# Performance work log

Hardware: AMD Instinct MI355X
Metric: run time of the kernel (lower is better)

## Reference

```python
import jax, jax.numpy as jnp
import numpy as np
import math

NUM_BANDS = 16
BINS = 1024
CROPSIZE = 1024
BATCH = 4


def setup_inputs() -> dict:
    key = jax.random.key(0)
    ks = jax.random.split(key, 10)
    s = 1.0 / math.sqrt(BINS)
    return {
        "x": jax.random.normal(ks[0], (BATCH, CROPSIZE, BINS), jnp.float32),
        "Wq": jax.random.normal(ks[1], (BINS, BINS), jnp.float32) * s,
        "bq": jax.random.normal(ks[2], (BINS,), jnp.float32) * 0.02,
        "Wk": jax.random.normal(ks[3], (BINS, BINS), jnp.float32) * s,
        "bk": jax.random.normal(ks[4], (BINS,), jnp.float32) * 0.02,
        "Wv": jax.random.normal(ks[5], (BINS, BINS), jnp.float32) * s,
        "bv": jax.random.normal(ks[6], (BINS,), jnp.float32) * 0.02,
        "Wo": jax.random.normal(ks[7], (BINS, BINS), jnp.float32) * s,
        "bo": jax.random.normal(ks[8], (BINS,), jnp.float32) * 0.02,
        "er": jax.random.normal(ks[9], (BINS // NUM_BANDS, CROPSIZE), jnp.float32),
    }


def reference(x, Wq, bq, Wk, bk, Wv, bv, Wo, bo, er):
    b, w, c = x.shape
    h = NUM_BANDS
    d = c // h
    # Linear projections (torch Linear: x @ W.T + b)
    q = (jnp.einsum("bwc,oc->bwo", x, Wq) + bq).reshape(b, w, h, d).transpose(0, 2, 1, 3)  # [b,h,w,d]
    k = (jnp.einsum("bwc,oc->bwo", x, Wk) + bk).reshape(b, w, h, d).transpose(0, 2, 1, 3)  # [b,h,w,d]
    v = (jnp.einsum("bwc,oc->bwo", x, Wv) + bv).reshape(b, w, h, d).transpose(0, 2, 1, 3)  # [b,h,w,d]
    # relative-position bias via skew trick
    qe = jnp.einsum("bhwd,dc->bhwc", q, er)  # [b,h,w,cropsize]
    qe = jnp.pad(qe, ((0, 0), (0, 0), (0, 0), (1, 0)))  # pad last dim on left -> [b,h,w,crop+1]
    p = jnp.swapaxes(qe, 2, 3)[:, :, 1:, :]  # [b,h,crop,w] == [b,h,w,w] since crop==w
    qk = (jnp.einsum("bhwd,bhud->bhwu", q, k) + p) / math.sqrt(c)
    a = jax.nn.softmax(qk, axis=-1)
    av = jnp.einsum("bhwu,bhud->bhwd", a, v).transpose(0, 2, 1, 3).reshape(b, w, c)
    return jnp.einsum("bwc,oc->bwo", av, Wo) + bo
```

## Files before the change

kernel.cpp:

```cpp
#include <hip/hip_runtime.h>
#include <stdint.h>

typedef __attribute__((ext_vector_type(8))) short   short8;
typedef __attribute__((ext_vector_type(8))) __bf16  bf16x8;
typedef __attribute__((ext_vector_type(4))) float   floatx4;

__device__ __forceinline__ float bf2f(uint16_t h) {
    union { uint32_t u; float f; } v; v.u = ((uint32_t)h) << 16; return v.f;
}
__device__ __forceinline__ uint16_t f2bf(float f) {
    union { float f; uint32_t u; } v; v.f = f;
    uint32_t u = v.u;
    u += 0x7FFFu + ((u >> 16) & 1u);
    return (uint16_t)(u >> 16);
}
__device__ __forceinline__ floatx4 mfma16(short8 a, short8 b, floatx4 c) {
    return __builtin_amdgcn_mfma_f32_16x16x32_bf16(
        __builtin_bit_cast(bf16x8, a), __builtin_bit_cast(bf16x8, b), c, 0, 0, 0);
}
__device__ __forceinline__ void gll16(const short* g, short* l) {
    __builtin_amdgcn_global_load_lds(
        (const __attribute__((address_space(1))) uint32_t*)g,
        (__attribute__((address_space(3))) uint32_t*)l, 16, 0, 0);
}

__global__ void conv_all(
    const float* __restrict__ x,
    const float* __restrict__ Wq, const float* __restrict__ Wk,
    const float* __restrict__ Wv, const float* __restrict__ Wo,
    const float* __restrict__ bq, const float* __restrict__ bk,
    const float* __restrict__ bv, const float* __restrict__ bo,
    const float* __restrict__ er,
    short* __restrict__ xb, short* __restrict__ Wb,
    short* __restrict__ ball, short* __restrict__ ErT)
{
    int blk = blockIdx.x, tid = threadIdx.x;
    if (blk < 4096) {
        int i = blk * 256 + tid;
        float4 v = ((const float4*)x)[i];
        ((short4*)xb)[i] = make_short4((short)f2bf(v.x), (short)f2bf(v.y),
                                       (short)f2bf(v.z), (short)f2bf(v.w));
    } else if (blk < 8192) {
        int rel = blk - 4096;
        int wsel = rel >> 10;
        int i = (rel & 1023) * 256 + tid;
        const float* W = (wsel == 0) ? Wq : (wsel == 1) ? Wk : (wsel == 2) ? Wv : Wo;
        float4 v = ((const float4*)W)[i];
        ((short4*)(Wb + ((size_t)wsel << 20)))[i] =
            make_short4((short)f2bf(v.x), (short)f2bf(v.y),
                        (short)f2bf(v.z), (short)f2bf(v.w));
    } else if (blk < 8448) {
        int idx = (blk - 8192) * 256 + tid;
        int w = idx >> 6, d = idx & 63;
        ErT[idx] = (short)f2bf(er[d * 1024 + w]);
    } else {
        int idx = (blk - 8448) * 256 + tid;
        int sel = idx >> 10, j = idx & 1023;
        const float* s = (sel == 0) ? bq : (sel == 1) ? bk : (sel == 2) ? bv : bo;
        ball[idx] = (short)f2bf(s[j]);
    }
}

__device__ __forceinline__ void gemm_body(
    const short* __restrict__ A, const short* __restrict__ Wt,
    const short* __restrict__ bias, short* __restrict__ dst,
    float* __restrict__ dstf, int variant)
{
    __shared__ short As[128 * 64];
    __shared__ short Bs[128 * 64];
    const int tid  = threadIdx.x;
    const int wid  = tid >> 6;
    const int lane = tid & 63;
    const int m0 = blockIdx.x * 128;
    const int n0 = blockIdx.y * 128;
    const int wm = (wid >> 1) * 64;
    const int wn = (wid & 1) * 64;
    const int lrow = lane & 15;
    const int quad = lane >> 4;
    const int srow = lane >> 3;
    const int sscol = (((lane & 7) ^ (srow & 7)) << 3);
    const int rx = lrow & 7;

    floatx4 acc[4][4];
#pragma unroll
    for (int r = 0; r < 4; ++r)
#pragma unroll
        for (int c = 0; c < 4; ++c) acc[r][c] = (floatx4){0.f, 0.f, 0.f, 0.f};

    for (int k0 = 0; k0 < 1024; k0 += 64) {
#pragma unroll
        for (int i = 0; i < 4; ++i) {
            int q = wid * 4 + i;
            gll16(A + (size_t)(m0 + q * 8 + srow) * 1024 + k0 + sscol,
                  &As[q * 512 + lane * 8]);
        }
#pragma unroll
        for (int i = 0; i < 4; ++i) {
            int q = wid * 4 + i;
            gll16(Wt + (size_t)(n0 + q * 8 + srow) * 1024 + k0 + sscol,
                  &Bs[q * 512 + lane * 8]);
        }
        __syncthreads();
#pragma unroll
        for (int ks = 0; ks < 2; ++ks) {
            short8 af[4], bfr[4];
#pragma unroll
            for (int r = 0; r < 4; ++r)
                af[r] = *(const short8*)&As[(wm + r * 16 + lrow) * 64 +
                                            (((ks * 4 + quad) ^ rx) << 3)];
#pragma unroll
            for (int c = 0; c < 4; ++c)
                bfr[c] = *(const short8*)&Bs[(wn + c * 16 + lrow) * 64 +
                                             (((ks * 4 + quad) ^ rx) << 3)];
#pragma unroll
            for (int r = 0; r < 4; ++r)
#pragma unroll
                for (int c = 0; c < 4; ++c)
                    acc[r][c] = mfma16(af[r], bfr[c], acc[r][c]);
        }
        __syncthreads();
    }

#pragma unroll
    for (int c = 0; c < 4; ++c) {
        int col = n0 + wn + c * 16 + lrow;
        float bv = bf2f((uint16_t)bias[col]);
#pragma unroll
        for (int r = 0; r < 4; ++r) {
#pragma unroll
            for (int g = 0; g < 4; ++g) {
                int m = m0 + wm + r * 16 + quad * 4 + g;
                float fv = acc[r][c][g] + bv;
                if (variant == 3) {
                    dstf[(size_t)m * 1024 + col] = fv;
                } else if (variant == 2) {
                    int bh = (m >> 10) * 16 + (col >> 6);
                    dst[(size_t)bh * 65536 + (size_t)(col & 63) * 1024 + (m & 1023)] =
                        (short)f2bf(fv);
                } else {
                    int bh = (m >> 10) * 16 + (col >> 6);
                    dst[(size_t)bh * 65536 + (size_t)(m & 1023) * 64 + (col & 63)] =
                        (short)f2bf(fv);
                }
            }
        }
    }
}

__global__ __launch_bounds__(256) void out_gemm(
    const short* __restrict__ AV, const short* __restrict__ Wo,
    const short* __restrict__ bo, float* __restrict__ out)
{
    gemm_body(AV, Wo, bo, nullptr, out, 3);
}

#define VM7  asm volatile("s_waitcnt vmcnt(7)" ::: "memory")
#define VM6  asm volatile("s_waitcnt vmcnt(6)" ::: "memory")
#define VM0  asm volatile("s_waitcnt vmcnt(0)" ::: "memory")
#define BARR asm volatile("s_barrier" ::: "memory")

__device__ __forceinline__ void stage_unit(const short* src, short* region, int tid)
{
    const int row  = tid >> 3;
    const int scol = (((tid & 7) ^ (row & 7)) << 3);
    gll16(src + (size_t)row * 1024 + scol, region + tid * 8);
}

#define SAU(buf, u) (As + (buf) * 16384 + (u) * 4096)
#define SBU(buf, u) (Bs + (buf) * 12288 + (u) * 4096)
#define STG_A(buf, u, kt) stage_unit(Asrc + (size_t)(u) * 65536 + (size_t)(kt) * 64, SAU(buf, u), tid)
#define STG_B(buf, u, kt) stage_unit(Bsrc + (size_t)(u) * 65536 + (size_t)(kt) * 64, SBU(buf, u), tid)

#define RD_A(buf) do { \
    _Pragma("unroll") for (int fr_ = 0; fr_ < 8; ++fr_) { \
        const short* p_ = SAU(buf, wm * 2 + (fr_ >> 2)) + ((fr_ & 3) * 16 + lrow) * 64; \
        _Pragma("unroll") for (int ks_ = 0; ks_ < 2; ++ks_) \
            a[fr_][ks_] = *(const short8*)&p_[((ks_ * 4 + quad) ^ rx) << 3]; \
    } } while (0)

#define RD_B(buf, c) do { \
    const short* p_ = SBU(buf, c) + (wn * 16 + lrow) * 64; \
    _Pragma("unroll") for (int ks_ = 0; ks_ < 2; ++ks_) \
        bb[ks_] = *(const short8*)&p_[((ks_ * 4 + quad) ^ rx) << 3]; \
    } while (0)

#define MFMA_PH(c) do { \
    __builtin_amdgcn_s_setprio(1); \
    _Pragma("unroll") for (int ks_ = 0; ks_ < 2; ++ks_) \
        _Pragma("unroll") for (int fr_ = 0; fr_ < 8; ++fr_) \
            acc[fr_][c] = mfma16(a[fr_][ks_], bb[ks_], acc[fr_][c]); \
    __builtin_amdgcn_s_setprio(0); \
    } while (0)

__global__ __launch_bounds__(512, 2) void qkv_gemm192(
    const short* __restrict__ x, const short* __restrict__ Wb,
    const short* __restrict__ ball,
    short* __restrict__ Qb, short* __restrict__ Kb, short* __restrict__ Vb)
{
    extern __shared__ short lds[];
    short* As = lds;
    short* Bs = lds + 32768;
    const int tid  = threadIdx.x;
    const int wid  = tid >> 6;
    const int lane = tid & 63;
    const int wm   = wid >> 2;
    const int wn   = wid & 3;
    const int lrow = lane & 15;
    const int quad = lane >> 4;
    const int rx   = lrow & 7;
    const int bid  = blockIdx.x;
    const int swz  = (bid & 7) * 32 + (bid >> 3);
    const int mi   = swz & 15, ni = swz >> 4;
    const int m0   = mi * 256, n0 = ni * 192;
    const short* Asrc = x  + (size_t)m0 * 1024;
    const short* Bsrc = Wb + (size_t)n0 * 1024;

    floatx4 acc[8][3];
#pragma unroll
    for (int r = 0; r < 8; ++r)
#pragma unroll
        for (int c = 0; c < 3; ++c) acc[r][c] = (floatx4){0.f, 0.f, 0.f, 0.f};

    short8 a[8][2], bb[2];

    STG_A(0, 0, 0); STG_A(0, 1, 0); STG_A(0, 2, 0); STG_A(0, 3, 0);
    STG_B(0, 0, 0); STG_B(0, 1, 0); STG_B(0, 2, 0);
    STG_A(1, 0, 1); STG_A(1, 1, 1); STG_A(1, 2, 1); STG_A(1, 3, 1);
    STG_B(1, 0, 1); STG_B(1, 1, 1);
    VM6; BARR;

#pragma unroll 1
    for (int i = 0; i < 7; ++i) {
        const int t1 = 2 * i + 1, s0 = 2 * i + 2, s1 = 2 * i + 3;
        STG_B(1, 2, t1);
        VM7; BARR;
        RD_A(0); RD_B(0, 0); MFMA_PH(0);
        BARR;
        STG_A(0, 0, s0); STG_A(0, 1, s0); STG_B(0, 0, s0);
        BARR; RD_B(0, 1); MFMA_PH(1); BARR;
        STG_A(0, 2, s0); STG_A(0, 3, s0); STG_B(0, 1, s0);
        BARR; RD_B(0, 2); MFMA_PH(2); BARR;
        STG_B(0, 2, s0);
        VM7; BARR;
        RD_A(1); RD_B(1, 0); MFMA_PH(0);
        BARR;
        STG_A(1, 0, s1); STG_A(1, 1, s1); STG_B(1, 0, s1);
        BARR; RD_B(1, 1); MFMA_PH(1); BARR;
        STG_A(1, 2, s1); STG_A(1, 3, s1); STG_B(1, 1, s1);
        BARR; RD_B(1, 2); MFMA_PH(2); BARR;
    }

    STG_B(1, 2, 15);
    VM7; BARR;
    RD_A(0); RD_B(0, 0); MFMA_PH(0);
    RD_B(0, 1); MFMA_PH(1);
    RD_B(0, 2); MFMA_PH(2);
    VM0; BARR;
    RD_A(1); RD_B(1, 0); MFMA_PH(0);
    RD_B(1, 1); MFMA_PH(1);
    RD_B(1, 2); MFMA_PH(2);

#pragma unroll
    for (int fc = 0; fc < 3; ++fc) {
        int col = n0 + fc * 64 + wn * 16 + lrow;
        int z   = col >> 10;
        int c1  = col & 1023;
        short* dst = (z == 0) ? Qb : (z == 1) ? Kb : Vb;
        float bv = bf2f((uint16_t)ball[col]);
#pragma unroll
        for (int fr = 0; fr < 8; ++fr) {
#pragma unroll
            for (int g = 0; g < 4; ++g) {
                int m = m0 + wm * 128 + fr * 16 + quad * 4 + g;
                float fv = acc[fr][fc][g] + bv;
                int bh = (m >> 10) * 16 + (c1 >> 6);
                if (z == 2)
                    dst[(size_t)bh * 65536 + (size_t)(c1 & 63) * 1024 + (m & 1023)] =
                        (short)f2bf(fv);
                else
                    dst[(size_t)bh * 65536 + (size_t)(m & 1023) * 64 + (c1 & 63)] =
                        (short)f2bf(fv);
            }
        }
    }
}

#define PSTR 72
__global__ __launch_bounds__(512, 4) void attn_kernel(
    const short* __restrict__ Q, const short* __restrict__ K,
    const short* __restrict__ Vt, const short* __restrict__ ErT,
    short* __restrict__ AV)
{
    __shared__ short smem[33792];
    short* Ks  = smem;
    short* Qks = smem + 8192;
    short* Vs  = smem + 16384;
    short* Ps  = smem + 24576;
    float* oaccS = (float*)smem;
    float* lrunS = ((float*)smem) + 128 * 65;

    const int tid  = threadIdx.x;
    const int wid  = tid >> 6;
    const int lane = tid & 63;
    const int rg   = wid >> 1;
    const int cg   = wid & 1;
    const int lrow = lane & 15;
    const int quad = lane >> 4;
    const int lk   = quad * 8;
    const int srow = lane >> 3;
    const int sscol = (((lane & 7) ^ (srow & 7)) << 3);
    const int rx = lrow & 7;
    const int h = blockIdx.x, b = blockIdx.y;
    const int bh = b * 16 + h;
    const int i0 = blockIdx.z * 128;
    const short* Qbh = Q  + (size_t)bh * 65536;
    const short* Kbh = K  + (size_t)bh * 65536;
    const short* Vbh = Vt + (size_t)bh * 65536;

    short8 qa[2][4];
#pragma unroll
    for (int m = 0; m < 2; ++m) {
        int row = i0 + rg * 32 + m * 16 + lrow;
#pragma unroll
        for (int kk = 0; kk < 2; ++kk) {
            qa[m][kk]     = *(const short8*)&Qbh[(size_t)row * 64 + kk * 32 + lk];
            qa[m][kk + 2] = *(const short8*)&ErT[(size_t)row * 64 + kk * 32 + lk];
        }
    }

    float lrun[2][4];
    floatx4 oacc[2][4];
#pragma unroll
    for (int m = 0; m < 2; ++m) {
#pragma unroll
        for (int g = 0; g < 4; ++g) lrun[m][g] = 0.f;
#pragma unroll
        for (int c = 0; c < 4; ++c) oacc[m][c] = (floatx4){0.f, 0.f, 0.f, 0.f};
    }

    gll16(Kbh + (size_t)(wid * 8 + srow) * 64 + sscol,    Ks  + wid * 512 + lane * 8);
    gll16(Qbh + (size_t)(wid * 8 + srow) * 64 + sscol,    Qks + wid * 512 + lane * 8);
    gll16(Vbh + (size_t)(wid * 8 + srow) * 1024 + sscol,  Vs  + wid * 512 + lane * 8);

    const float sc2 = 1.44269504088896f / 32.0f;

    for (int jt = 0; jt < 16; ++jt) {
        const int cur = jt & 1;
        __syncthreads();

        if (jt < 15) {
            int j1 = (jt + 1) * 64;
            gll16(Kbh + (size_t)(j1 + wid * 8 + srow) * 64 + sscol,    Ks  + (cur ^ 1) * 4096 + wid * 512 + lane * 8);
            gll16(Qbh + (size_t)(j1 + wid * 8 + srow) * 64 + sscol,    Qks + (cur ^ 1) * 4096 + wid * 512 + lane * 8);
            gll16(Vbh + (size_t)(wid * 8 + srow) * 1024 + j1 + sscol,  Vs  + (cur ^ 1) * 4096 + wid * 512 + lane * 8);
        }

        floatx4 s[2][2];
#pragma unroll
        for (int m = 0; m < 2; ++m)
#pragma unroll
            for (int c = 0; c < 2; ++c) s[m][c] = (floatx4){0.f, 0.f, 0.f, 0.f};
#pragma unroll
        for (int kk = 0; kk < 4; ++kk) {
            short8 kb[2];
            const short* src = ((kk < 2) ? Ks : Qks) + cur * 4096;
            const int kl = kk & 1;
#pragma unroll
            for (int c = 0; c < 2; ++c)
                kb[c] = *(const short8*)&src[(cg * 32 + c * 16 + lrow) * 64 +
                                             (((kl * 4 + quad) ^ rx) << 3)];
#pragma unroll
            for (int m = 0; m < 2; ++m)
#pragma unroll
                for (int c = 0; c < 2; ++c)
                    s[m][c] = mfma16(qa[m][kk], kb[c], s[m][c]);
        }

#pragma unroll
        for (int m = 0; m < 2; ++m)
#pragma unroll
            for (int c = 0; c < 2; ++c)
#pragma unroll
                for (int g = 0; g < 4; ++g)
                    s[m][c][g] = exp2f(s[m][c][g] * sc2);
#pragma unroll
        for (int m = 0; m < 2; ++m)
#pragma unroll
            for (int g = 0; g < 4; ++g)
                lrun[m][g] += s[m][0][g] + s[m][1][g];

#pragma unroll
        for (int m = 0; m < 2; ++m)
#pragma unroll
            for (int c = 0; c < 2; ++c)
#pragma unroll
                for (int g = 0; g < 4; ++g)
                    Ps[(rg * 32 + m * 16 + quad * 4 + g) * PSTR + cg * 32 + c * 16 + lrow] =
                        (short)f2bf(s[m][c][g]);
        __asm__ __volatile__("" ::: "memory");

        {
            short8 pa[2], vb[4];
#pragma unroll
            for (int m = 0; m < 2; ++m)
                pa[m] = *(const short8*)&Ps[(rg * 32 + m * 16 + lrow) * PSTR + cg * 32 + lk];
#pragma unroll
            for (int c = 0; c < 4; ++c)
                vb[c] = *(const short8*)&Vs[cur * 4096 + (c * 16 + lrow) * 64 +
                                            (((cg * 4 + quad) ^ rx) << 3)];
#pragma unroll
            for (int m = 0; m < 2; ++m)
#pragma unroll
                for (int c = 0; c < 4; ++c)
                    oacc[m][c] = mfma16(pa[m], vb[c], oacc[m][c]);
        }
    }

#pragma unroll
    for (int m = 0; m < 2; ++m)
#pragma unroll
        for (int g = 0; g < 4; ++g) {
            float r = lrun[m][g];
#pragma unroll
            for (int d = 1; d < 16; d <<= 1) r += __shfl_xor(r, d, 64);
            lrun[m][g] = r;
        }

    __syncthreads();
    if (cg == 0) {
#pragma unroll
        for (int m = 0; m < 2; ++m) {
#pragma unroll
            for (int c = 0; c < 4; ++c)
#pragma unroll
                for (int g = 0; g < 4; ++g)
                    oaccS[(rg * 32 + m * 16 + quad * 4 + g) * 65 + c * 16 + lrow] =
                        oacc[m][c][g];
            if (lrow == 0)
#pragma unroll
                for (int g = 0; g < 4; ++g)
                    lrunS[rg * 32 + m * 16 + quad * 4 + g] = lrun[m][g];
        }
    }
    __syncthreads();
    if (cg == 1) {
#pragma unroll
        for (int m = 0; m < 2; ++m)
#pragma unroll
            for (int g = 0; g < 4; ++g) {
                int row = rg * 32 + m * 16 + quad * 4 + g;
                float lt = lrun[m][g] + lrunS[row];
#pragma unroll
                for (int c = 0; c < 4; ++c) {
                    float tot = oacc[m][c][g] + oaccS[row * 65 + c * 16 + lrow];
                    AV[((size_t)b * 1024 + i0 + row) * 1024 + h * 64 + c * 16 + lrow] =
                        (short)f2bf(tot / lt);
                }
            }
    }
}

extern "C" void kernel_launch(void* const* d_in, const int* in_sizes, int n_in,
                              void* d_out, int out_size, void* d_ws, size_t ws_size,
                              hipStream_t stream) {
    const float* x  = (const float*)d_in[0];
    const float* Wq = (const float*)d_in[1];
    const float* bq = (const float*)d_in[2];
    const float* Wk = (const float*)d_in[3];
    const float* bk = (const float*)d_in[4];
    const float* Wv = (const float*)d_in[5];
    const float* bv = (const float*)d_in[6];
    const float* Wo = (const float*)d_in[7];
    const float* bo = (const float*)d_in[8];
    const float* er = (const float*)d_in[9];
    float* out = (float*)d_out;

    const size_t M1 = 1u << 20;
    short* ws   = (short*)d_ws;
    short* xb   = (short*)d_out;
    short* Qb   = ws;
    short* Kb   = ws + 4 * M1;
    short* Vb   = ws + 8 * M1;
    short* AVb  = ws + 12 * M1;
    short* Wb   = ws + 16 * M1;
    short* ball = ws + 20 * M1;
    short* ErT  = ws + 20 * M1 + 4096;

    static bool attr_done = false;
    if (!attr_done) {
        hipFuncSetAttribute((const void*)qkv_gemm192,
                            hipFuncAttributeMaxDynamicSharedMemorySize, 114688);
        attr_done = true;
    }

    hipLaunchKernelGGL(conv_all, dim3(8464), dim3(256), 0, stream,
                       x, Wq, Wk, Wv, Wo, bq, bk, bv, bo, er, xb, Wb, ball, ErT);
    hipLaunchKernelGGL(qkv_gemm192, dim3(256), dim3(512), 114688, stream,
                       xb, Wb, ball, Qb, Kb, Vb);
    hipLaunchKernelGGL(attn_kernel, dim3(16, 4, 8), dim3(512), 0, stream,
                       Qb, Kb, Vb, ErT, AVb);
    hipLaunchKernelGGL(out_gemm, dim3(32, 8), dim3(256), 0, stream,
                       AVb, Wb + 3 * M1, ball + 3072, out);
}
```

Measured before the change: 201.5 us.

## Replace fine-grained interleaved QKV GEMM pipeline with simple two-phase double buffering

The QKV projection GEMM used to stage sub-tiles of the next K-step between individual MFMA phases, guarded by partial vmcnt waits and many barriers. It now issues all seven loads for the next K-tile at the start of each iteration, runs all three MFMA phases on the current buffer, then waits for every load and barriers once. This cuts barrier and waitcnt overhead and simplifies scheduling. In exchange it loses the finer overlap of loads with compute and uses a full vmcnt(0) drain each iteration, which can expose memory latency.

```diff
diff --git a/kernel.cpp b/kernel.cpp
--- a/kernel.cpp
+++ b/kernel.cpp
@@ -154,8 +154,6 @@
     gemm_body(AV, Wo, bo, nullptr, out, 3);
 }
 
-#define VM7  asm volatile("s_waitcnt vmcnt(7)" ::: "memory")
-#define VM6  asm volatile("s_waitcnt vmcnt(6)" ::: "memory")
 #define VM0  asm volatile("s_waitcnt vmcnt(0)" ::: "memory")
 #define BARR asm volatile("s_barrier" ::: "memory")
 
@@ -170,6 +168,9 @@
 #define SBU(buf, u) (Bs + (buf) * 12288 + (u) * 4096)
 #define STG_A(buf, u, kt) stage_unit(Asrc + (size_t)(u) * 65536 + (size_t)(kt) * 64, SAU(buf, u), tid)
 #define STG_B(buf, u, kt) stage_unit(Bsrc + (size_t)(u) * 65536 + (size_t)(kt) * 64, SBU(buf, u), tid)
+#define STG7(buf, kt) do { \
+    STG_A(buf, 0, kt); STG_A(buf, 1, kt); STG_A(buf, 2, kt); STG_A(buf, 3, kt); \
+    STG_B(buf, 0, kt); STG_B(buf, 1, kt); STG_B(buf, 2, kt); } while (0)
 
 #define RD_A(buf) do { \
     _Pragma("unroll") for (int fr_ = 0; fr_ < 8; ++fr_) { \
@@ -192,7 +193,7 @@
     __builtin_amdgcn_s_setprio(0); \
     } while (0)
 
-__global__ __launch_bounds__(512, 2) void qkv_gemm192(
+__global__ __launch_bounds__(512, 2) void qkv_gemm2ph(
     const short* __restrict__ x, const short* __restrict__ Wb,
     const short* __restrict__ ball,
     short* __restrict__ Qb, short* __restrict__ Kb, short* __restrict__ Vb)
@@ -223,42 +224,19 @@
 
     short8 a[8][2], bb[2];
 
-    STG_A(0, 0, 0); STG_A(0, 1, 0); STG_A(0, 2, 0); STG_A(0, 3, 0);
-    STG_B(0, 0, 0); STG_B(0, 1, 0); STG_B(0, 2, 0);
-    STG_A(1, 0, 1); STG_A(1, 1, 1); STG_A(1, 2, 1); STG_A(1, 3, 1);
-    STG_B(1, 0, 1); STG_B(1, 1, 1);
-    VM6; BARR;
-
-#pragma unroll 1
-    for (int i = 0; i < 7; ++i) {
-        const int t1 = 2 * i + 1, s0 = 2 * i + 2, s1 = 2 * i + 3;
-        STG_B(1, 2, t1);
-        VM7; BARR;
-        RD_A(0); RD_B(0, 0); MFMA_PH(0);
-        BARR;
-        STG_A(0, 0, s0); STG_A(0, 1, s0); STG_B(0, 0, s0);
-        BARR; RD_B(0, 1); MFMA_PH(1); BARR;
-        STG_A(0, 2, s0); STG_A(0, 3, s0); STG_B(0, 1, s0);
-        BARR; RD_B(0, 2); MFMA_PH(2); BARR;
-        STG_B(0, 2, s0);
-        VM7; BARR;
-        RD_A(1); RD_B(1, 0); MFMA_PH(0);
-        BARR;
-        STG_A(1, 0, s1); STG_A(1, 1, s1); STG_B(1, 0, s1);
-        BARR; RD_B(1, 1); MFMA_PH(1); BARR;
-        STG_A(1, 2, s1); STG_A(1, 3, s1); STG_B(1, 1, s1);
-        BARR; RD_B(1, 2); MFMA_PH(2); BARR;
-    }
-
-    STG_B(1, 2, 15);
-    VM7; BARR;
-    RD_A(0); RD_B(0, 0); MFMA_PH(0);
-    RD_B(0, 1); MFMA_PH(1);
-    RD_B(0, 2); MFMA_PH(2);
+    STG7(0, 0);
     VM0; BARR;
-    RD_A(1); RD_B(1, 0); MFMA_PH(0);
-    RD_B(1, 1); MFMA_PH(1);
-    RD_B(1, 2); MFMA_PH(2);
+
+#pragma unroll 2
+    for (int t = 0; t < 16; ++t) {
+        const int cur = t & 1;
+        if (t < 15) STG7(cur ^ 1, t + 1);
+        RD_A(cur);
+        RD_B(cur, 0); MFMA_PH(0);
+        RD_B(cur, 1); MFMA_PH(1);
+        RD_B(cur, 2); MFMA_PH(2);
+        VM0; BARR;
+    }
 
 #pragma unroll
     for (int fc = 0; fc < 3; ++fc) {
@@ -488,14 +466,14 @@
 
     static bool attr_done = false;
     if (!attr_done) {
-        hipFuncSetAttribute((const void*)qkv_gemm192,
+        hipFuncSetAttribute((const void*)qkv_gemm2ph,
                             hipFuncAttributeMaxDynamicSharedMemorySize, 114688);
         attr_done = true;
     }
 
     hipLaunchKernelGGL(conv_all, dim3(8464), dim3(256), 0, stream,
                        x, Wq, Wk, Wv, Wo, bq, bk, bv, bo, er, xb, Wb, ball, ErT);
-    hipLaunchKernelGGL(qkv_gemm192, dim3(256), dim3(512), 114688, stream,
+    hipLaunchKernelGGL(qkv_gemm2ph, dim3(256), dim3(512), 114688, stream,
                        xb, Wb, ball, Qb, Kb, Vb);
     hipLaunchKernelGGL(attn_kernel, dim3(16, 4, 8), dim3(512), 0, stream,
                        Qb, Kb, Vb, ErT, AVb);
```

Result: no change. 203.7 us (+1.1%).
